# Kernel optimization log

Hardware: AMD Instinct MI355X
Metric: run time of the kernel (lower is better)

The kernel has to match this reference:

```python
import jax, jax.numpy as jnp
import numpy as np
import math

BS, N = 32, 2048
INPUT_SIZE, HIDDEN, NUM_LAYERS = 128, 64, 4
ALPHA, LAMDA = 0.1, 1.0
EPS = 1e-5
EDGE_P = 0.01


def setup_inputs() -> dict:
    key = jax.random.key(0)
    ks = jax.random.split(key, 6)
    x = jax.random.normal(ks[0], (BS, N, INPUT_SIZE), jnp.float32)
    adj = (jax.random.uniform(ks[1], (BS, N, N)) < EDGE_P).astype(jnp.float32)
    adj = adj * (1.0 - jnp.eye(N, dtype=jnp.float32))  # no pre-existing self loops
    proj_w = jax.random.normal(ks[2], (INPUT_SIZE, HIDDEN), jnp.float32) * (1.0 / math.sqrt(INPUT_SIZE))
    proj_b = jnp.zeros((HIDDEN,), jnp.float32)
    ln_g = jnp.ones((NUM_LAYERS, HIDDEN), jnp.float32)
    ln_b = jnp.zeros((NUM_LAYERS, HIDDEN), jnp.float32)
    conv_w = jax.random.normal(ks[3], (NUM_LAYERS, HIDDEN, HIDDEN), jnp.float32) * (1.0 / math.sqrt(HIDDEN))
    head_w = jax.random.normal(ks[4], (HIDDEN, 1), jnp.float32) * (1.0 / math.sqrt(HIDDEN))
    head_b = jnp.zeros((1,), jnp.float32)
    return dict(x=x, adj=adj, proj_w=proj_w, proj_b=proj_b, ln_g=ln_g, ln_b=ln_b,
                conv_w=conv_w, head_w=head_w, head_b=head_b)


def _layer_norm(h, g, b):
    mu = h.mean(-1, keepdims=True)
    var = ((h - mu) ** 2).mean(-1, keepdims=True)
    return (h - mu) * jax.lax.rsqrt(var + EPS) * g + b


def _gcn_norm(adj):
    # A_hat = D^{-1/2} (A + I) D^{-1/2}; only the nonzero pattern of adj is used,
    # matching adj.nonzero() -> edge_index with unit edge weights + added self loops.
    a = (adj != 0).astype(adj.dtype) + jnp.eye(adj.shape[-1], dtype=adj.dtype)
    dinv = jax.lax.rsqrt(a.sum(-1))  # deg >= 1 thanks to self loops
    return a * dinv[:, :, None] * dinv[:, None, :]


def _forward(x, adj_hat, proj_w, proj_b, ln_g, ln_b, conv_w, head_w, head_b):
    h = x @ proj_w + proj_b  # [bs, N, hidden]
    for i in range(NUM_LAYERS):
        beta = math.log(LAMDA / (i + 1) + 1.0)  # GCNII identity-mapping strength
        # DeepGCNLayer block='res+': h_in -> norm -> act -> conv, then residual add
        z = jax.nn.relu(_layer_norm(h, ln_g[i], ln_b[i]))
        p = jnp.einsum('bij,bjd->bid', adj_hat, z)          # neighbor aggregation
        s = (1.0 - ALPHA) * p + ALPHA * z                   # initial residual (x0 = conv input)
        h = h + (1.0 - beta) * s + beta * (s @ conv_w[i])   # GCN2Conv out + res+ skip
    return h @ head_w + head_b  # [bs, N, 1]


def reference(x, adj, proj_w, proj_b, ln_g, ln_b, conv_w, head_w, head_b):
    return _forward(x, _gcn_norm(adj), proj_w, proj_b, ln_g, ln_b, conv_w, head_w, head_b)
```

## Files before the change

### kernel.cpp

```cpp
#include <hip/hip_runtime.h>
#include <math.h>

#define BS 32
#define N 2048
#define ROWS (BS * N)
#define IN 128
#define HID 64
#define K_CAP 80
#define EPS 1e-5f
#define ALPHA 0.1f

typedef float fx4 __attribute__((ext_vector_type(4)));

__global__ __launch_bounds__(256) void k_build(const float* __restrict__ adj,
                                               int* __restrict__ ell,
                                               int* __restrict__ cnt,
                                               float* __restrict__ dinv) {
    int lane = threadIdx.x & 63;
    int row  = blockIdx.x * 4 + (threadIdx.x >> 6);
    const fx4* arow = (const fx4*)(adj + (size_t)row * N);
    int* erow = ell + (size_t)row * K_CAP;
    int base = 0;
#pragma unroll
    for (int it = 0; it < N / 256; it++) {
        fx4 f = __builtin_nontemporal_load(&arow[it * 64 + lane]);
#pragma unroll
        for (int k = 0; k < 4; k++) {
            float v = f[k];
            unsigned long long m = __ballot(v != 0.0f);
            if (v != 0.0f) {
                int pos = base + __popcll(m & ((1ull << lane) - 1ull));
                if (pos < K_CAP) erow[pos] = it * 256 + lane * 4 + k;
            }
            base += __popcll(m);
        }
    }
    if (lane == 0) {
        cnt[row]  = base < K_CAP ? base : K_CAP;
        dinv[row] = rsqrtf((float)base + 1.0f);
    }
}

__global__ __launch_bounds__(256) void k_proj_ln(const float* __restrict__ x,
                                                 const float* __restrict__ w,
                                                 const float* __restrict__ b,
                                                 const float* __restrict__ g0,
                                                 const float* __restrict__ b0,
                                                 float* __restrict__ h,
                                                 float* __restrict__ z0) {
    __shared__ float sw[IN * HID];
    __shared__ float sx[4][IN];
    int tx = threadIdx.x;
    for (int i = tx; i < IN * HID; i += 256) sw[i] = w[i];
    int row0 = blockIdx.x * 4;
    if (tx < 128) {
        float4 v = *(const float4*)(x + (size_t)(row0 + (tx >> 5)) * IN + (tx & 31) * 4);
        *(float4*)&sx[tx >> 5][(tx & 31) * 4] = v;
    }
    __syncthreads();
    int c = tx & 63, r = tx >> 6;
    float acc = b[c];
#pragma unroll
    for (int k = 0; k < IN; k += 4) {
        float4 xa = *(const float4*)&sx[r][k];
        acc += xa.x * sw[(k + 0) * HID + c];
        acc += xa.y * sw[(k + 1) * HID + c];
        acc += xa.z * sw[(k + 2) * HID + c];
        acc += xa.w * sw[(k + 3) * HID + c];
    }
    size_t idx = (size_t)(row0 + r) * HID + c;
    h[idx] = acc;
    float sum = acc;
    for (int o = 32; o >= 1; o >>= 1) sum += __shfl_xor(sum, o);
    float mu = sum * (1.0f / 64.0f);
    float d  = acc - mu;
    float vs = d * d;
    for (int o = 32; o >= 1; o >>= 1) vs += __shfl_xor(vs, o);
    float rr = rsqrtf(vs * (1.0f / 64.0f) + EPS);
    float zz = d * rr * g0[c] + b0[c];
    z0[idx] = zz > 0.0f ? zz : 0.0f;
}

__global__ __launch_bounds__(256) void k_layer(
    float* __restrict__ h, const float* __restrict__ z_in,
    float* __restrict__ z_out,
    const int* __restrict__ ell, const int* __restrict__ cnt,
    const float* __restrict__ dinv, const float* __restrict__ w,
    const float* __restrict__ g_next, const float* __restrict__ b_next,
    float beta, int is_last,
    const float* __restrict__ head_w, const float* __restrict__ head_b,
    float* __restrict__ out) {
    __shared__ float sw[HID * HID];
    __shared__ float ss[16][HID];
    int tx = threadIdx.x;
    int lane = tx & 63, wid = tx >> 6;
    int p = lane & 15, q = lane >> 4;

    int bid = blockIdx.x;
    int swz = (bid & 7) * (int)(gridDim.x >> 3) + (bid >> 3);
    int row0 = swz * 16 + wid * 4;
    int jbase = row0 & ~(N - 1);

    for (int i = tx; i < HID * HID; i += 256) sw[i] = w[i];

    int   nn[4];
    float di[4];
    int   myidx[4];
    float myw[4];
    float4 zi4[4];
#pragma unroll
    for (int rr = 0; rr < 4; rr++) {
        int row = row0 + rr;
        nn[rr] = cnt[row];
        di[rr] = dinv[row];
        zi4[rr] = *(const float4*)(z_in + (size_t)row * HID + 4 * p);
        myidx[rr] = 0; myw[rr] = 0.0f;
        if (lane < nn[rr]) {
            myidx[rr] = ell[(size_t)row * K_CAP + lane];
            myw[rr]   = dinv[jbase + myidx[rr]];
        }
    }

#pragma unroll
    for (int rr = 0; rr < 4; rr++) {
        float4 acc = make_float4(0.0f, 0.0f, 0.0f, 0.0f);
        int nmain = nn[rr] < 64 ? nn[rr] : 64;
        int ntot  = (nmain + 3) & ~3;
        for (int t = q; t < ntot; t += 4) {
            int   j  = jbase + __shfl(myidx[rr], t);
            float wj = __shfl(myw[rr], t);
            float4 zj = *(const float4*)(z_in + (size_t)j * HID + 4 * p);
            acc.x += wj * zj.x; acc.y += wj * zj.y;
            acc.z += wj * zj.z; acc.w += wj * zj.w;
        }
        for (int t = 64 + q; t < nn[rr]; t += 4) {
            int   j  = jbase + ell[(size_t)(row0 + rr) * K_CAP + t];
            float wj = dinv[j];
            float4 zj = *(const float4*)(z_in + (size_t)j * HID + 4 * p);
            acc.x += wj * zj.x; acc.y += wj * zj.y;
            acc.z += wj * zj.z; acc.w += wj * zj.w;
        }
        acc.x += __shfl_xor(acc.x, 16); acc.y += __shfl_xor(acc.y, 16);
        acc.z += __shfl_xor(acc.z, 16); acc.w += __shfl_xor(acc.w, 16);
        acc.x += __shfl_xor(acc.x, 32); acc.y += __shfl_xor(acc.y, 32);
        acc.z += __shfl_xor(acc.z, 32); acc.w += __shfl_xor(acc.w, 32);
        float dd = di[rr];
        float4 s4;
        s4.x = (1.0f - ALPHA) * dd * (acc.x + dd * zi4[rr].x) + ALPHA * zi4[rr].x;
        s4.y = (1.0f - ALPHA) * dd * (acc.y + dd * zi4[rr].y) + ALPHA * zi4[rr].y;
        s4.z = (1.0f - ALPHA) * dd * (acc.z + dd * zi4[rr].z) + ALPHA * zi4[rr].z;
        s4.w = (1.0f - ALPHA) * dd * (acc.w + dd * zi4[rr].w) + ALPHA * zi4[rr].w;
        if (q == 0) *(float4*)&ss[wid * 4 + rr][4 * p] = s4;
    }
    __syncthreads();

#pragma unroll
    for (int rr = 0; rr < 4; rr++) {
        int row = row0 + rr;
        float mv = 0.0f;
#pragma unroll
        for (int k = 0; k < HID; k += 4) {
            float4 sk = *(const float4*)&ss[wid * 4 + rr][k];
            mv += sk.x * sw[(k + 0) * HID + lane];
            mv += sk.y * sw[(k + 1) * HID + lane];
            mv += sk.z * sw[(k + 2) * HID + lane];
            mv += sk.w * sw[(k + 3) * HID + lane];
        }
        float s_c = ss[wid * 4 + rr][lane];
        size_t idx = (size_t)row * HID + lane;
        float hn = __builtin_nontemporal_load(h + idx) +
                   (1.0f - beta) * s_c + beta * mv;
        if (!is_last) {
            __builtin_nontemporal_store(hn, h + idx);
            float sum = hn;
            for (int o = 32; o >= 1; o >>= 1) sum += __shfl_xor(sum, o);
            float mu = sum * (1.0f / 64.0f);
            float d  = hn - mu;
            float vs = d * d;
            for (int o = 32; o >= 1; o >>= 1) vs += __shfl_xor(vs, o);
            float rv = rsqrtf(vs * (1.0f / 64.0f) + EPS);
            float zz = d * rv * g_next[lane] + b_next[lane];
            z_out[idx] = zz > 0.0f ? zz : 0.0f;
        } else {
            float v = hn * head_w[lane];
            for (int o = 32; o >= 1; o >>= 1) v += __shfl_xor(v, o);
            if (lane == 0) out[row] = v + head_b[0];
        }
    }
}

extern "C" void kernel_launch(void* const* d_in, const int* in_sizes, int n_in,
                              void* d_out, int out_size, void* d_ws, size_t ws_size,
                              hipStream_t stream) {
    const float* x      = (const float*)d_in[0];
    const float* adj    = (const float*)d_in[1];
    const float* proj_w = (const float*)d_in[2];
    const float* proj_b = (const float*)d_in[3];
    const float* ln_g   = (const float*)d_in[4];
    const float* ln_b   = (const float*)d_in[5];
    const float* conv_w = (const float*)d_in[6];
    const float* head_w = (const float*)d_in[7];
    const float* head_b = (const float*)d_in[8];
    float* out = (float*)d_out;

    float* h    = (float*)d_ws;
    float* za   = h + (size_t)ROWS * HID;
    float* zb   = za + (size_t)ROWS * HID;
    float* dinv = zb + (size_t)ROWS * HID;
    int*   cnt  = (int*)(dinv + ROWS);
    int*   ell  = cnt + ROWS;

    dim3 blk(256);

    k_build<<<dim3(ROWS / 4), blk, 0, stream>>>(adj, ell, cnt, dinv);
    k_proj_ln<<<dim3(ROWS / 4), blk, 0, stream>>>(x, proj_w, proj_b, ln_g, ln_b, h, za);

    float* zin = za;
    float* zout = zb;
    for (int i = 0; i < 4; i++) {
        float beta = (float)log(1.0 / (double)(i + 1) + 1.0);
        int last = (i == 3);
        int gi = (i + 1) < 3 ? (i + 1) : 3;
        k_layer<<<dim3(ROWS / 16), blk, 0, stream>>>(h, zin, zout, ell, cnt, dinv,
                                                     conv_w + (size_t)i * HID * HID,
                                                     ln_g + gi * HID, ln_b + gi * HID,
                                                     beta, last, head_w, head_b, out);
        float* t = zin; zin = zout; zout = t;
    }
}
```

Before: 404.9 us.

## Split layer into LDS-cached SpMM and dense update kernels with precomputed edge weights

Each layer is split into two kernels. The first is a sparse aggregation kernel that stages a 16-column slice of one graph's z matrix (128 KB) in shared memory, so gathers read from LDS instead of global memory. The second is an update kernel that does the 64x64 matmul, residual, layernorm and head. Symmetric normalization weights are precomputed once per edge so the gather no longer has to look up dinv. The cost is extra launches, an s buffer written to and read back from global memory, and a 128 KB LDS tile per 512-thread block, which limits occupancy to one block per CU and gives only 256 blocks.

```diff
diff --git a/kernel.cpp b/kernel.cpp
--- a/kernel.cpp
+++ b/kernel.cpp
@@ -39,6 +39,23 @@
         cnt[row]  = base < K_CAP ? base : K_CAP;
         dinv[row] = rsqrtf((float)base + 1.0f);
     }
+}
+
+__global__ __launch_bounds__(256) void k_weights(const int* __restrict__ ell,
+                                                 const int* __restrict__ cnt,
+                                                 const float* __restrict__ dinv,
+                                                 float* __restrict__ wgt,
+                                                 float* __restrict__ dself) {
+    int lane = threadIdx.x & 63;
+    int row  = blockIdx.x * 4 + (threadIdx.x >> 6);
+    int jb   = row & ~(N - 1);
+    int n    = cnt[row];
+    float di = dinv[row];
+    for (int t = lane; t < n; t += 64) {
+        int j = ell[(size_t)row * K_CAP + t];
+        wgt[(size_t)row * K_CAP + t] = di * dinv[jb + j];
+    }
+    if (lane == 0) dself[row] = di * di;
 }
 
 __global__ __launch_bounds__(256) void k_proj_ln(const float* __restrict__ x,
@@ -81,11 +98,65 @@
     z0[idx] = zz > 0.0f ? zz : 0.0f;
 }
 
-__global__ __launch_bounds__(256) void k_layer(
-    float* __restrict__ h, const float* __restrict__ z_in,
-    float* __restrict__ z_out,
-    const int* __restrict__ ell, const int* __restrict__ cnt,
-    const float* __restrict__ dinv, const float* __restrict__ w,
+__global__ __launch_bounds__(512) void k_spmm(const float* __restrict__ z_in,
+                                              const int* __restrict__ ell,
+                                              const float* __restrict__ wgt,
+                                              const int* __restrict__ cnt,
+                                              const float* __restrict__ dself,
+                                              float* __restrict__ s) {
+    __shared__ float zc[N * 16];
+    int tx = threadIdx.x;
+    int bid = blockIdx.x;
+    int swz = (bid & 7) * 32 + (bid >> 3);
+    int b = swz >> 3, sub = swz & 7;
+    int half = sub & 1, chunk = sub >> 1;
+    int rowbase = b * N;
+    int cbase = chunk * 16;
+
+    for (int i = tx; i < N * 4; i += 512) {
+        int j = i >> 2, sb = i & 3;
+        float4 v = *(const float4*)(z_in + (size_t)(rowbase + j) * HID + cbase + sb * 4);
+        *(float4*)&zc[j * 16 + sb * 4] = v;
+    }
+    __syncthreads();
+
+    int lane = tx & 63, wid = tx >> 6;
+    int p = lane & 15, q = lane >> 4;
+    int r0 = rowbase + half * (N / 2) + wid * (N / 16);
+
+#pragma unroll 2
+    for (int rr = 0; rr < N / 16; rr++) {
+        int row = r0 + rr;
+        int n = cnt[row];
+        float ds = dself[row];
+        const int*   erow = ell + (size_t)row * K_CAP;
+        const float* wrow = wgt + (size_t)row * K_CAP;
+        int   idx = 0;
+        float w   = 0.0f;
+        if (lane < n) { idx = erow[lane]; w = wrow[lane]; }
+        float zi = zc[(row - rowbase) * 16 + p];
+        float acc = 0.0f;
+        int nm = n < 64 ? n : 64;
+        int ntot = (nm + 3) & ~3;
+        for (int t = q; t < ntot; t += 4) {
+            int   j  = __shfl(idx, t);
+            float wj = __shfl(w, t);
+            acc += wj * zc[j * 16 + p];
+        }
+        for (int t = 64 + q; t < n; t += 4) {
+            acc += wrow[t] * zc[erow[t] * 16 + p];
+        }
+        acc += __shfl_xor(acc, 16);
+        acc += __shfl_xor(acc, 32);
+        if (q == 0)
+            s[(size_t)row * HID + cbase + p] =
+                (1.0f - ALPHA) * (acc + ds * zi) + ALPHA * zi;
+    }
+}
+
+__global__ __launch_bounds__(256) void k_update(
+    float* __restrict__ h, const float* __restrict__ s,
+    float* __restrict__ z_out, const float* __restrict__ w,
     const float* __restrict__ g_next, const float* __restrict__ b_next,
     float beta, int is_last,
     const float* __restrict__ head_w, const float* __restrict__ head_b,
@@ -94,79 +165,30 @@
     __shared__ float ss[16][HID];
     int tx = threadIdx.x;
     int lane = tx & 63, wid = tx >> 6;
-    int p = lane & 15, q = lane >> 4;
-
     int bid = blockIdx.x;
     int swz = (bid & 7) * (int)(gridDim.x >> 3) + (bid >> 3);
-    int row0 = swz * 16 + wid * 4;
-    int jbase = row0 & ~(N - 1);
-
+    int row0 = swz * 16;
     for (int i = tx; i < HID * HID; i += 256) sw[i] = w[i];
-
-    int   nn[4];
-    float di[4];
-    int   myidx[4];
-    float myw[4];
-    float4 zi4[4];
+#pragma unroll
+    for (int i = 0; i < 4; i++) {
+        int r = wid * 4 + i;
+        ss[r][lane] = s[(size_t)(row0 + r) * HID + lane];
+    }
+    __syncthreads();
 #pragma unroll
     for (int rr = 0; rr < 4; rr++) {
-        int row = row0 + rr;
-        nn[rr] = cnt[row];
-        di[rr] = dinv[row];
-        zi4[rr] = *(const float4*)(z_in + (size_t)row * HID + 4 * p);
-        myidx[rr] = 0; myw[rr] = 0.0f;
-        if (lane < nn[rr]) {
-            myidx[rr] = ell[(size_t)row * K_CAP + lane];
-            myw[rr]   = dinv[jbase + myidx[rr]];
-        }
-    }
-
-#pragma unroll
-    for (int rr = 0; rr < 4; rr++) {
-        float4 acc = make_float4(0.0f, 0.0f, 0.0f, 0.0f);
-        int nmain = nn[rr] < 64 ? nn[rr] : 64;
-        int ntot  = (nmain + 3) & ~3;
-        for (int t = q; t < ntot; t += 4) {
-            int   j  = jbase + __shfl(myidx[rr], t);
-            float wj = __shfl(myw[rr], t);
-            float4 zj = *(const float4*)(z_in + (size_t)j * HID + 4 * p);
-            acc.x += wj * zj.x; acc.y += wj * zj.y;
-            acc.z += wj * zj.z; acc.w += wj * zj.w;
-        }
-        for (int t = 64 + q; t < nn[rr]; t += 4) {
-            int   j  = jbase + ell[(size_t)(row0 + rr) * K_CAP + t];
-            float wj = dinv[j];
-            float4 zj = *(const float4*)(z_in + (size_t)j * HID + 4 * p);
-            acc.x += wj * zj.x; acc.y += wj * zj.y;
-            acc.z += wj * zj.z; acc.w += wj * zj.w;
-        }
-        acc.x += __shfl_xor(acc.x, 16); acc.y += __shfl_xor(acc.y, 16);
-        acc.z += __shfl_xor(acc.z, 16); acc.w += __shfl_xor(acc.w, 16);
-        acc.x += __shfl_xor(acc.x, 32); acc.y += __shfl_xor(acc.y, 32);
-        acc.z += __shfl_xor(acc.z, 32); acc.w += __shfl_xor(acc.w, 32);
-        float dd = di[rr];
-        float4 s4;
-        s4.x = (1.0f - ALPHA) * dd * (acc.x + dd * zi4[rr].x) + ALPHA * zi4[rr].x;
-        s4.y = (1.0f - ALPHA) * dd * (acc.y + dd * zi4[rr].y) + ALPHA * zi4[rr].y;
-        s4.z = (1.0f - ALPHA) * dd * (acc.z + dd * zi4[rr].z) + ALPHA * zi4[rr].z;
-        s4.w = (1.0f - ALPHA) * dd * (acc.w + dd * zi4[rr].w) + ALPHA * zi4[rr].w;
-        if (q == 0) *(float4*)&ss[wid * 4 + rr][4 * p] = s4;
-    }
-    __syncthreads();
-
-#pragma unroll
-    for (int rr = 0; rr < 4; rr++) {
-        int row = row0 + rr;
+        int r = wid * 4 + rr;
+        int row = row0 + r;
         float mv = 0.0f;
 #pragma unroll
         for (int k = 0; k < HID; k += 4) {
-            float4 sk = *(const float4*)&ss[wid * 4 + rr][k];
+            float4 sk = *(const float4*)&ss[r][k];
             mv += sk.x * sw[(k + 0) * HID + lane];
             mv += sk.y * sw[(k + 1) * HID + lane];
             mv += sk.z * sw[(k + 2) * HID + lane];
             mv += sk.w * sw[(k + 3) * HID + lane];
         }
-        float s_c = ss[wid * 4 + rr][lane];
+        float s_c = ss[r][lane];
         size_t idx = (size_t)row * HID + lane;
         float hn = __builtin_nontemporal_load(h + idx) +
                    (1.0f - beta) * s_c + beta * mv;
@@ -203,16 +225,20 @@
     const float* head_b = (const float*)d_in[8];
     float* out = (float*)d_out;
 
-    float* h    = (float*)d_ws;
-    float* za   = h + (size_t)ROWS * HID;
-    float* zb   = za + (size_t)ROWS * HID;
-    float* dinv = zb + (size_t)ROWS * HID;
-    int*   cnt  = (int*)(dinv + ROWS);
-    int*   ell  = cnt + ROWS;
+    float* h     = (float*)d_ws;
+    float* za    = h + (size_t)ROWS * HID;
+    float* zb    = za + (size_t)ROWS * HID;
+    float* sbuf  = zb + (size_t)ROWS * HID;
+    float* dinv  = sbuf + (size_t)ROWS * HID;
+    float* dself = dinv + ROWS;
+    int*   cnt   = (int*)(dself + ROWS);
+    int*   ell   = cnt + ROWS;
+    float* wgt   = (float*)(ell + (size_t)ROWS * K_CAP);
 
     dim3 blk(256);
 
     k_build<<<dim3(ROWS / 4), blk, 0, stream>>>(adj, ell, cnt, dinv);
+    k_weights<<<dim3(ROWS / 4), blk, 0, stream>>>(ell, cnt, dinv, wgt, dself);
     k_proj_ln<<<dim3(ROWS / 4), blk, 0, stream>>>(x, proj_w, proj_b, ln_g, ln_b, h, za);
 
     float* zin = za;
@@ -221,10 +247,11 @@
         float beta = (float)log(1.0 / (double)(i + 1) + 1.0);
         int last = (i == 3);
         int gi = (i + 1) < 3 ? (i + 1) : 3;
-        k_layer<<<dim3(ROWS / 16), blk, 0, stream>>>(h, zin, zout, ell, cnt, dinv,
-                                                     conv_w + (size_t)i * HID * HID,
-                                                     ln_g + gi * HID, ln_b + gi * HID,
-                                                     beta, last, head_w, head_b, out);
+        k_spmm<<<dim3(BS * 8), dim3(512), 0, stream>>>(zin, ell, wgt, cnt, dself, sbuf);
+        k_update<<<dim3(ROWS / 16), blk, 0, stream>>>(h, sbuf, zout,
+                                                      conv_w + (size_t)i * HID * HID,
+                                                      ln_g + gi * HID, ln_b + gi * HID,
+                                                      beta, last, head_w, head_b, out);
         float* t = zin; zin = zout; zout = t;
     }
 }
```

Measured after the change: 841.8 us. 2.08x slower.
